# Optimization experiments

Measured on AMD Instinct MI355X. Metric: run time of the kernel, lower is better.

Reference implementation:

```python
import jax, jax.numpy as jnp
import numpy as np
from jax import lax

N_CLASSES = 10
N_EXPERTS = 45  # 10 choose 2
EPS = 1e-5

# lookup table: (i1, i2) with i1 < i2 -> flat expert id (matches nested loop order)
_tbl = np.zeros((N_CLASSES, N_CLASSES), dtype=np.int32)
_k = 0
for _i1 in range(N_CLASSES):
    for _i2 in range(_i1 + 1, N_CLASSES):
        _tbl[_i1, _i2] = _k
        _k += 1
PAIR_TABLE = jnp.asarray(_tbl)


def _downscale(x):
    # AvgPool2d(3, stride=3) on 28x28 -> 9x9 (floor: uses top-left 27x27)
    B = x.shape[0]
    return x[:, :, :27, :27].reshape(B, 1, 9, 3, 9, 3).mean(axis=(3, 5))


def _bn_eval(h, gamma, beta, mean, var):
    scale = gamma * lax.rsqrt(var + EPS)
    return h * scale[None, :, None, None] + (beta - mean * scale)[None, :, None, None]


def _stage1(x, w1, b1, g1, be1, m1, v1, fcw1, fcb1):
    xd = _downscale(x)                                         # [B,1,9,9]
    h = lax.conv_general_dilated(xd, w1, (1, 1), 'VALID',
                                 dimension_numbers=('NCHW', 'OIHW', 'NCHW'))
    h = h + b1[None, :, None, None]                            # [B,20,7,7]
    h = _bn_eval(h, g1, be1, m1, v1)
    h = jax.nn.relu(h)
    B = h.shape[0]
    h = h[:, :, :6, :6].reshape(B, 20, 3, 2, 3, 2).max(axis=(3, 5))  # maxpool2 -> [B,20,3,3]
    h = h.reshape(B, 180)
    return h @ fcw1.T + fcb1                                   # [B,10] raw logits


def reference(x, w1, b1, g1, be1, m1, v1, fcw1, fcb1,
              w2, b2, g2, be2, m2, v2, fcw2, fcb2):
    B = x.shape[0]
    logits1 = _stage1(x, w1, b1, g1, be1, m1, v1, fcw1, fcb1)  # [B,10]
    ls1 = jax.nn.log_softmax(logits1, axis=1)

    # routing: top-2 class indices, sorted ascending, -> pairwise expert id
    top2 = jnp.sort(jnp.argsort(ls1, axis=1)[:, -2:], axis=1)  # [B,2]
    idx0, idx1 = top2[:, 0], top2[:, 1]
    eid = PAIR_TABLE[idx0, idx1]                               # [B]

    # stage 2 (TinyNet2) with per-example gathered expert params
    xd = _downscale(x)                                         # [B,1,9,9]
    # extract 5x5 conv patches (valid, stride 1): output spatial 5x5
    patches = jnp.stack([xd[:, 0, i:i + 5, j:j + 5]
                         for i in range(5) for j in range(5)], axis=1)  # [B,25,5,5]
    Wsel = w2.reshape(N_EXPERTS, 15, 25)[eid]                  # [B,15,25]
    h = jnp.einsum('bkhw,bok->bohw', patches, Wsel) + b2[eid][:, :, None, None]  # [B,15,5,5]
    scale = (g2 * lax.rsqrt(v2 + EPS))[eid]                    # [B,15]
    shift = (be2 - m2 * g2 * lax.rsqrt(v2 + EPS))[eid]
    h = h * scale[:, :, None, None] + shift[:, :, None, None]
    h = jax.nn.relu(h)
    h = h[:, :, :4, :4].reshape(B, 15, 2, 2, 2, 2).max(axis=(3, 5))  # [B,15,2,2]
    feat = h.reshape(B, 60)
    s2 = jnp.einsum('bf,bof->bo', feat, fcw2[eid]) + fcb2[eid]  # [B,2]

    # combine: scatter the two expert logits into the routed columns
    rows = jnp.arange(B)
    out = jnp.full((B, N_CLASSES), -100.0, dtype=logits1.dtype)
    out = out.at[rows, idx0].set(s2[:, 0]).at[rows, idx1].set(s2[:, 1])
    # eval-mode bypass: use stage1 raw logits if max log-prob > 0.3
    use1 = jnp.max(ls1, axis=1) > 0.3
    out = jnp.where(use1[:, None], logits1, out)
    out = jax.nn.log_softmax(out, axis=1)
    return (logits1, out)


def setup_inputs() -> dict:
    key = jax.random.key(0)
    ks = jax.random.split(key, 18)
    B = 65536
    s = 0.1
    return {
        'x': jax.random.normal(ks[0], (B, 1, 28, 28), dtype=jnp.float32),
        # stage1 (TinyNet, 20 kernels, k=3)
        'w1': jax.random.normal(ks[1], (20, 1, 3, 3), dtype=jnp.float32) * s,
        'b1': jax.random.normal(ks[2], (20,), dtype=jnp.float32) * s,
        'g1': jax.random.normal(ks[3], (20,), dtype=jnp.float32) * s + 1.0,
        'be1': jax.random.normal(ks[4], (20,), dtype=jnp.float32) * s,
        'm1': jax.random.normal(ks[5], (20,), dtype=jnp.float32) * s,
        'v1': jax.random.uniform(ks[6], (20,), dtype=jnp.float32) + 0.5,
        'fcw1': jax.random.normal(ks[7], (10, 180), dtype=jnp.float32) * s,
        'fcb1': jax.random.normal(ks[8], (10,), dtype=jnp.float32) * s,
        # 45 stacked stage2 experts (TinyNet2, 15 kernels, k=5)
        'w2': jax.random.normal(ks[9], (45, 15, 1, 5, 5), dtype=jnp.float32) * s,
        'b2': jax.random.normal(ks[10], (45, 15), dtype=jnp.float32) * s,
        'g2': jax.random.normal(ks[11], (45, 15), dtype=jnp.float32) * s + 1.0,
        'be2': jax.random.normal(ks[12], (45, 15), dtype=jnp.float32) * s,
        'm2': jax.random.normal(ks[13], (45, 15), dtype=jnp.float32) * s,
        'v2': jax.random.uniform(ks[14], (45, 15), dtype=jnp.float32) + 0.5,
        'fcw2': jax.random.normal(ks[15], (45, 2, 60), dtype=jnp.float32) * s,
        'fcb2': jax.random.normal(ks[16], (45, 2), dtype=jnp.float32) * s,
    }
```

## Files before the change

kernel.cpp:

```cpp
#include <hip/hip_runtime.h>
#include <cmath>

#define EPSF 1e-5f


__global__ __launch_bounds__(256) void setup_tables(
    const float* __restrict__ w1, const float* __restrict__ b1,
    const float* __restrict__ g1, const float* __restrict__ be1,
    const float* __restrict__ m1, const float* __restrict__ v1,
    const float* __restrict__ w2, const float* __restrict__ b2,
    const float* __restrict__ g2, const float* __restrict__ be2,
    const float* __restrict__ m2, const float* __restrict__ v2,
    const float* __restrict__ fcw2, const float* __restrict__ fcb2,
    float* __restrict__ ws)
{
  const int t  = blockIdx.x * blockDim.x + threadIdx.x;
  const int nt = gridDim.x * blockDim.x;
  float* W2F  = ws;
  float* B2F  = W2F + 18900;
  float* FC2  = W2F + 19576;
  float* FCB2 = FC2 + 5400;
  float* W1F  = FCB2 + 90;
  float* B1F  = W1F + 180;

  for (int idx = t; idx < 18900; idx += nt) {
    int kk = idx & 3, rest = idx >> 2;
    int e = rest % 45, ok4 = rest / 45;
    int k4 = ok4 % 7, o = ok4 / 7;
    int k = k4 * 4 + kk;
    float s = g2[e*15+o] / sqrtf(v2[e*15+o] + EPSF);
    W2F[idx] = (k < 25) ? w2[(e*15+o)*25 + k] * s : 0.0f;
  }
  for (int idx = t; idx < 675; idx += nt) {
    int e = idx % 45, o = idx / 45;
    float s = g2[e*15+o] / sqrtf(v2[e*15+o] + EPSF);
    B2F[idx] = b2[e*15+o]*s + be2[e*15+o] - m2[e*15+o]*s;
  }
  for (int idx = t; idx < 5400; idx += nt) {
    int kk = idx & 3, rest = idx >> 2;
    int e = rest % 45, t2 = rest / 45;
    int f4 = t2 % 15, oo = t2 / 15;
    FC2[idx] = fcw2[(e*2+oo)*60 + f4*4 + kk];
  }
  for (int idx = t; idx < 90; idx += nt) {
    int e = idx % 45, oo = idx / 45;
    FCB2[idx] = fcb2[e*2+oo];
  }
  for (int idx = t; idx < 180; idx += nt) {
    int ch = idx / 9;
    float s = g1[ch] / sqrtf(v1[ch] + EPSF);
    W1F[idx] = w1[idx] * s;
  }
  for (int idx = t; idx < 20; idx += nt) {
    float s = g1[idx] / sqrtf(v1[idx] + EPSF);
    B1F[idx] = b1[idx]*s + be1[idx] - m1[idx]*s;
  }
}

#define GETC(arr, k) ((k)%4==0 ? arr[(k)/4].x : (k)%4==1 ? arr[(k)/4].y : \
                      (k)%4==2 ? arr[(k)/4].z : arr[(k)/4].w)

__global__ __launch_bounds__(64, 1) void fused_k(
    const float* __restrict__ x,
    const float* __restrict__ ws,
    const float* __restrict__ fcw1, const float* __restrict__ fcb1,
    float* __restrict__ out, int B)
{
  const int b = blockIdx.x * 64 + threadIdx.x;
  if (b >= B) return;

  const float* W2F  = ws;
  const float* B2F  = W2F + 18900;
  const float* FC2  = W2F + 19576;
  const float* FCB2 = FC2 + 5400;
  const float* W1F  = FCB2 + 90;
  const float* B1F  = W1F + 180;

  float xd[81];
  const float* xb = x + (size_t)b * 784;
  #pragma unroll
  for (int r = 0; r < 9; r++) {
    float4 rowv[3][7];
    #pragma unroll
    for (int dr = 0; dr < 3; dr++) {
      const float4* rv = reinterpret_cast<const float4*>(xb + (3*r + dr) * 28);
      #pragma unroll
      for (int q = 0; q < 7; q++) rowv[dr][q] = rv[q];
    }
    #pragma unroll
    for (int c = 0; c < 9; c++) {
      float s = 0.0f;
      #pragma unroll
      for (int dr = 0; dr < 3; dr++)
        s += GETC(rowv[dr], 3*c) + GETC(rowv[dr], 3*c+1) + GETC(rowv[dr], 3*c+2);
      xd[r*9 + c] = s * (1.0f / 9.0f);
    }
  }

  float logits[10];
  #pragma unroll
  for (int c = 0; c < 10; c++) logits[c] = fcb1[c];

  #pragma unroll 1
  for (int ch = 0; ch < 20; ch++) {
    float w[9];
    #pragma unroll
    for (int k = 0; k < 9; k++) w[k] = W1F[ch*9 + k];
    float bb = B1F[ch];
    float feat[9];
    #pragma unroll
    for (int pr = 0; pr < 3; pr++) {
      #pragma unroll
      for (int pc = 0; pc < 3; pc++) {
        float c00 = bb, c01 = bb, c10 = bb, c11 = bb;
        #pragma unroll
        for (int dr = 0; dr < 3; dr++) {
          #pragma unroll
          for (int dc = 0; dc < 3; dc++) {
            float wk = w[dr*3 + dc];
            c00 = fmaf(xd[(2*pr+0+dr)*9 + 2*pc+0+dc], wk, c00);
            c01 = fmaf(xd[(2*pr+0+dr)*9 + 2*pc+1+dc], wk, c01);
            c10 = fmaf(xd[(2*pr+1+dr)*9 + 2*pc+0+dc], wk, c10);
            c11 = fmaf(xd[(2*pr+1+dr)*9 + 2*pc+1+dc], wk, c11);
          }
        }
        feat[pr*3+pc] = fmaxf(fmaxf(fmaxf(c00, c01), fmaxf(c10, c11)), 0.0f);
      }
    }
    #pragma unroll
    for (int c = 0; c < 10; c++) {
      float acc = logits[c];
      #pragma unroll
      for (int p = 0; p < 9; p++)
        acc = fmaf(feat[p], fcw1[c*180 + ch*9 + p], acc);
      logits[c] = acc;
    }
  }

  int i1 = 0; float v1m = logits[0];
  #pragma unroll
  for (int c = 1; c < 10; c++) { if (logits[c] >= v1m) { v1m = logits[c]; i1 = c; } }
  int i2 = 0; float v2m = -3.0e38f;
  #pragma unroll
  for (int c = 0; c < 10; c++) { if (c != i1 && logits[c] >= v2m) { v2m = logits[c]; i2 = c; } }
  int idx0 = i1 < i2 ? i1 : i2;
  int idx1 = i1 < i2 ? i2 : i1;
  int eid  = 8*idx0 - (idx0*(idx0-1))/2 + idx1 - 1;

  float mx = v1m;
  float sume = 0.0f;
  #pragma unroll
  for (int c = 0; c < 10; c++) sume += expf(logits[c] - mx);
  bool use1 = (-logf(sume)) > 0.3f;

  const float4* W2F4 = reinterpret_cast<const float4*>(W2F);
  const float4* FC24 = reinterpret_cast<const float4*>(FC2);

  float s2a = FCB2[eid], s2b = FCB2[45 + eid];

  float4 wv[7], fa, fb; float bias;
  #pragma unroll
  for (int k4 = 0; k4 < 7; k4++) wv[k4] = W2F4[k4*45 + eid];
  bias = B2F[eid];
  fa = FC24[eid];
  fb = FC24[15*45 + eid];

  #pragma unroll 1
  for (int o = 0; o < 15; o++) {
    float4 nwv[7], nfa, nfb; float nbias;
    if (o < 14) {
      #pragma unroll
      for (int k4 = 0; k4 < 7; k4++) nwv[k4] = W2F4[((o+1)*7 + k4)*45 + eid];
      nbias = B2F[(o+1)*45 + eid];
      nfa = FC24[(o+1)*45 + eid];
      nfb = FC24[(15 + o+1)*45 + eid];
    }
    float feat0 = 0.f, feat1 = 0.f, feat2 = 0.f, feat3 = 0.f;
    #pragma unroll
    for (int ph = 0; ph < 2; ph++) {
      #pragma unroll
      for (int pw = 0; pw < 2; pw++) {
        float c00 = bias, c01 = bias, c10 = bias, c11 = bias;
        #pragma unroll
        for (int i = 0; i < 5; i++) {
          #pragma unroll
          for (int j = 0; j < 5; j++) {
            float wk = GETC(wv, i*5 + j);
            c00 = fmaf(xd[(2*ph+0+i)*9 + 2*pw+0+j], wk, c00);
            c01 = fmaf(xd[(2*ph+0+i)*9 + 2*pw+1+j], wk, c01);
            c10 = fmaf(xd[(2*ph+1+i)*9 + 2*pw+0+j], wk, c10);
            c11 = fmaf(xd[(2*ph+1+i)*9 + 2*pw+1+j], wk, c11);
          }
        }
        float f = fmaxf(fmaxf(fmaxf(c00, c01), fmaxf(c10, c11)), 0.0f);
        if (ph == 0 && pw == 0) feat0 = f;
        else if (ph == 0)       feat1 = f;
        else if (pw == 0)       feat2 = f;
        else                    feat3 = f;
      }
    }
    s2a = fmaf(feat0, fa.x, fmaf(feat1, fa.y, fmaf(feat2, fa.z, fmaf(feat3, fa.w, s2a))));
    s2b = fmaf(feat0, fb.x, fmaf(feat1, fb.y, fmaf(feat2, fb.z, fmaf(feat3, fb.w, s2b))));
    if (o < 14) {
      #pragma unroll
      for (int k4 = 0; k4 < 7; k4++) wv[k4] = nwv[k4];
      bias = nbias; fa = nfa; fb = nfb;
    }
  }

  float o10[10];
  #pragma unroll
  for (int c = 0; c < 10; c++) {
    float v = -100.0f;
    v = (c == idx0) ? s2a : v;
    v = (c == idx1) ? s2b : v;
    o10[c] = use1 ? logits[c] : v;
  }
  float m2x = o10[0];
  #pragma unroll
  for (int c = 1; c < 10; c++) m2x = fmaxf(m2x, o10[c]);
  float se2 = 0.0f;
  #pragma unroll
  for (int c = 0; c < 10; c++) se2 += expf(o10[c] - m2x);
  float lse2 = m2x + logf(se2);

  size_t base = (size_t)b * 10;
  #pragma unroll
  for (int c = 0; c < 10; c++) out[base + c] = logits[c];
  #pragma unroll
  for (int c = 0; c < 10; c++) out[(size_t)B*10 + base + c] = o10[c] - lse2;
}

extern "C" void kernel_launch(void* const* d_in, const int* in_sizes, int n_in,
                              void* d_out, int out_size, void* d_ws, size_t ws_size,
                              hipStream_t stream) {
  const float* x    = (const float*)d_in[0];
  const float* w1   = (const float*)d_in[1];
  const float* b1   = (const float*)d_in[2];
  const float* g1   = (const float*)d_in[3];
  const float* be1  = (const float*)d_in[4];
  const float* m1   = (const float*)d_in[5];
  const float* v1   = (const float*)d_in[6];
  const float* fcw1 = (const float*)d_in[7];
  const float* fcb1 = (const float*)d_in[8];
  const float* w2   = (const float*)d_in[9];
  const float* b2   = (const float*)d_in[10];
  const float* g2   = (const float*)d_in[11];
  const float* be2  = (const float*)d_in[12];
  const float* m2   = (const float*)d_in[13];
  const float* v2   = (const float*)d_in[14];
  const float* fcw2 = (const float*)d_in[15];
  const float* fcb2 = (const float*)d_in[16];
  float* out = (float*)d_out;
  float* ws  = (float*)d_ws;
  const int B = in_sizes[0] / 784;

  setup_tables<<<80, 256, 0, stream>>>(w1, b1, g1, be1, m1, v1,
                                       w2, b2, g2, be2, m2, v2, fcw2, fcb2, ws);
  fused_k<<<(B + 63)/64, 64, 0, stream>>>(x, ws, fcw1, fcb1, out, B);
}
```

Before: 369.8 us.

## Split each sample across four lanes with shared-memory downscale and shuffle reductions

Each sample is now handled by four threads instead of one. The threads share the input downscale through LDS, split the stage-1 conv channels and the stage-2 expert output channels, and combine partial logits with xor shuffles. The fc1 weights are re-laid out in setup so they can be read with float4 loads, and the downscaled image is trimmed to the 8x8 region actually used. This is meant to cut per-thread register pressure and serial latency and to give the launch more waves. In exchange it duplicates the routing and softmax work across the four lanes and adds a block barrier.

```diff
diff --git a/kernel.cpp b/kernel.cpp
--- a/kernel.cpp
+++ b/kernel.cpp
@@ -3,6 +3,12 @@
 
 #define EPSF 1e-5f
 
+#define OFF_B2F   18900
+#define OFF_FC2   19576
+#define OFF_FCB2  24976
+#define OFF_W1P   25068
+#define OFF_FCW1R 25308
+#define OFF_B1F   27468
 
 __global__ __launch_bounds__(256) void setup_tables(
     const float* __restrict__ w1, const float* __restrict__ b1,
@@ -12,16 +18,18 @@
     const float* __restrict__ g2, const float* __restrict__ be2,
     const float* __restrict__ m2, const float* __restrict__ v2,
     const float* __restrict__ fcw2, const float* __restrict__ fcb2,
+    const float* __restrict__ fcw1,
     float* __restrict__ ws)
 {
   const int t  = blockIdx.x * blockDim.x + threadIdx.x;
   const int nt = gridDim.x * blockDim.x;
-  float* W2F  = ws;
-  float* B2F  = W2F + 18900;
-  float* FC2  = W2F + 19576;
-  float* FCB2 = FC2 + 5400;
-  float* W1F  = FCB2 + 90;
-  float* B1F  = W1F + 180;
+  float* W2F   = ws;
+  float* B2F   = ws + OFF_B2F;
+  float* FC2   = ws + OFF_FC2;
+  float* FCB2  = ws + OFF_FCB2;
+  float* W1P   = ws + OFF_W1P;
+  float* FCW1R = ws + OFF_FCW1R;
+  float* B1F   = ws + OFF_B1F;
 
   for (int idx = t; idx < 18900; idx += nt) {
     int kk = idx & 3, rest = idx >> 2;
@@ -46,10 +54,15 @@
     int e = idx % 45, oo = idx / 45;
     FCB2[idx] = fcb2[e*2+oo];
   }
-  for (int idx = t; idx < 180; idx += nt) {
-    int ch = idx / 9;
+  for (int idx = t; idx < 240; idx += nt) {
+    int j = idx % 12, ch = idx / 12;
     float s = g1[ch] / sqrtf(v1[ch] + EPSF);
-    W1F[idx] = w1[idx] * s;
+    W1P[idx] = (j < 9) ? w1[ch*9 + j] * s : 0.0f;
+  }
+  for (int idx = t; idx < 2160; idx += nt) {
+    int c = idx % 12, r2 = idx / 12;
+    int pp = r2 % 9, ch = r2 / 9;
+    FCW1R[idx] = (c < 10) ? fcw1[c*180 + ch*9 + pp] : 0.0f;
   }
   for (int idx = t; idx < 20; idx += nt) {
     float s = g1[idx] / sqrtf(v1[idx] + EPSF);
@@ -60,53 +73,76 @@
 #define GETC(arr, k) ((k)%4==0 ? arr[(k)/4].x : (k)%4==1 ? arr[(k)/4].y : \
                       (k)%4==2 ? arr[(k)/4].z : arr[(k)/4].w)
 
-__global__ __launch_bounds__(64, 1) void fused_k(
+__global__ __launch_bounds__(256, 3) void fused_k(
     const float* __restrict__ x,
     const float* __restrict__ ws,
-    const float* __restrict__ fcw1, const float* __restrict__ fcb1,
+    const float* __restrict__ fcb1,
     float* __restrict__ out, int B)
 {
-  const int b = blockIdx.x * 64 + threadIdx.x;
-  if (b >= B) return;
-
-  const float* W2F  = ws;
-  const float* B2F  = W2F + 18900;
-  const float* FC2  = W2F + 19576;
-  const float* FCB2 = FC2 + 5400;
-  const float* W1F  = FCB2 + 90;
-  const float* B1F  = W1F + 180;
-
-  float xd[81];
-  const float* xb = x + (size_t)b * 784;
-  #pragma unroll
-  for (int r = 0; r < 9; r++) {
-    float4 rowv[3][7];
+  __shared__ float xds[64 * 68];
+
+  const int t  = threadIdx.x;
+  const int p  = t & 3;
+  const int sl = t >> 2;
+  const int b  = blockIdx.x * 64 + sl;
+  const bool valid = (b < B);
+
+  const float* W2F   = ws;
+  const float* B2F   = ws + OFF_B2F;
+  const float* FC2   = ws + OFF_FC2;
+  const float* FCB2  = ws + OFF_FCB2;
+  const float* W1P   = ws + OFF_W1P;
+  const float* FCW1R = ws + OFF_FCW1R;
+  const float* B1F   = ws + OFF_B1F;
+
+  if (valid) {
+    const float* xb = x + (size_t)b * 784;
     #pragma unroll
-    for (int dr = 0; dr < 3; dr++) {
-      const float4* rv = reinterpret_cast<const float4*>(xb + (3*r + dr) * 28);
-      #pragma unroll
-      for (int q = 0; q < 7; q++) rowv[dr][q] = rv[q];
-    }
-    #pragma unroll
-    for (int c = 0; c < 9; c++) {
-      float s = 0.0f;
-      #pragma unroll
-      for (int dr = 0; dr < 3; dr++)
-        s += GETC(rowv[dr], 3*c) + GETC(rowv[dr], 3*c+1) + GETC(rowv[dr], 3*c+2);
-      xd[r*9 + c] = s * (1.0f / 9.0f);
-    }
+    for (int ri = 0; ri < 2; ri++) {
+      const int r = 2*p + ri;
+      float4 rowv[3][6];
+      #pragma unroll
+      for (int dr = 0; dr < 3; dr++) {
+        const float4* rv = reinterpret_cast<const float4*>(xb + (3*r + dr) * 28);
+        #pragma unroll
+        for (int q = 0; q < 6; q++) rowv[dr][q] = rv[q];
+      }
+      float d[8];
+      #pragma unroll
+      for (int c = 0; c < 8; c++) {
+        float s = 0.0f;
+        #pragma unroll
+        for (int dr = 0; dr < 3; dr++)
+          s += GETC(rowv[dr], 3*c) + GETC(rowv[dr], 3*c+1) + GETC(rowv[dr], 3*c+2);
+        d[c] = s * (1.0f / 9.0f);
+      }
+      float4* dst = reinterpret_cast<float4*>(&xds[sl*68 + r*8]);
+      dst[0] = make_float4(d[0], d[1], d[2], d[3]);
+      dst[1] = make_float4(d[4], d[5], d[6], d[7]);
+    }
+  }
+  __syncthreads();
+
+  float xd[64];
+  #pragma unroll
+  for (int r = 0; r < 8; r++) {
+    const float4* src = reinterpret_cast<const float4*>(&xds[sl*68 + r*8]);
+    float4 a = src[0], bq = src[1];
+    xd[r*8+0]=a.x;  xd[r*8+1]=a.y;  xd[r*8+2]=a.z;  xd[r*8+3]=a.w;
+    xd[r*8+4]=bq.x; xd[r*8+5]=bq.y; xd[r*8+6]=bq.z; xd[r*8+7]=bq.w;
   }
 
   float logits[10];
   #pragma unroll
-  for (int c = 0; c < 10; c++) logits[c] = fcb1[c];
+  for (int c = 0; c < 10; c++) logits[c] = 0.0f;
 
   #pragma unroll 1
-  for (int ch = 0; ch < 20; ch++) {
-    float w[9];
-    #pragma unroll
-    for (int k = 0; k < 9; k++) w[k] = W1F[ch*9 + k];
-    float bb = B1F[ch];
+  for (int ci = 0; ci < 5; ci++) {
+    const int ch = p*5 + ci;
+    const float4* wp = reinterpret_cast<const float4*>(W1P + ch*12);
+    float4 w0 = wp[0], w1v = wp[1], w2v = wp[2];
+    const float w_[9] = {w0.x,w0.y,w0.z,w0.w,w1v.x,w1v.y,w1v.z,w1v.w,w2v.x};
+    const float bb = B1F[ch];
     float feat[9];
     #pragma unroll
     for (int pr = 0; pr < 3; pr++) {
@@ -117,24 +153,40 @@
         for (int dr = 0; dr < 3; dr++) {
           #pragma unroll
           for (int dc = 0; dc < 3; dc++) {
-            float wk = w[dr*3 + dc];
-            c00 = fmaf(xd[(2*pr+0+dr)*9 + 2*pc+0+dc], wk, c00);
-            c01 = fmaf(xd[(2*pr+0+dr)*9 + 2*pc+1+dc], wk, c01);
-            c10 = fmaf(xd[(2*pr+1+dr)*9 + 2*pc+0+dc], wk, c10);
-            c11 = fmaf(xd[(2*pr+1+dr)*9 + 2*pc+1+dc], wk, c11);
+            float wk = w_[dr*3 + dc];
+            c00 = fmaf(xd[(2*pr+0+dr)*8 + 2*pc+0+dc], wk, c00);
+            c01 = fmaf(xd[(2*pr+0+dr)*8 + 2*pc+1+dc], wk, c01);
+            c10 = fmaf(xd[(2*pr+1+dr)*8 + 2*pc+0+dc], wk, c10);
+            c11 = fmaf(xd[(2*pr+1+dr)*8 + 2*pc+1+dc], wk, c11);
           }
         }
         feat[pr*3+pc] = fmaxf(fmaxf(fmaxf(c00, c01), fmaxf(c10, c11)), 0.0f);
       }
     }
     #pragma unroll
-    for (int c = 0; c < 10; c++) {
-      float acc = logits[c];
-      #pragma unroll
-      for (int p = 0; p < 9; p++)
-        acc = fmaf(feat[p], fcw1[c*180 + ch*9 + p], acc);
-      logits[c] = acc;
-    }
+    for (int pp = 0; pp < 9; pp++) {
+      const float4* f4 = reinterpret_cast<const float4*>(FCW1R + (ch*9 + pp)*12);
+      float4 f0 = f4[0], f1 = f4[1], f2 = f4[2];
+      const float fv = feat[pp];
+      logits[0] = fmaf(fv, f0.x, logits[0]);
+      logits[1] = fmaf(fv, f0.y, logits[1]);
+      logits[2] = fmaf(fv, f0.z, logits[2]);
+      logits[3] = fmaf(fv, f0.w, logits[3]);
+      logits[4] = fmaf(fv, f1.x, logits[4]);
+      logits[5] = fmaf(fv, f1.y, logits[5]);
+      logits[6] = fmaf(fv, f1.z, logits[6]);
+      logits[7] = fmaf(fv, f1.w, logits[7]);
+      logits[8] = fmaf(fv, f2.x, logits[8]);
+      logits[9] = fmaf(fv, f2.y, logits[9]);
+    }
+  }
+
+  #pragma unroll
+  for (int c = 0; c < 10; c++) {
+    float v = logits[c];
+    v += __shfl_xor(v, 1);
+    v += __shfl_xor(v, 2);
+    logits[c] = v + fcb1[c];
   }
 
   int i1 = 0; float v1m = logits[0];
@@ -143,70 +195,62 @@
   int i2 = 0; float v2m = -3.0e38f;
   #pragma unroll
   for (int c = 0; c < 10; c++) { if (c != i1 && logits[c] >= v2m) { v2m = logits[c]; i2 = c; } }
-  int idx0 = i1 < i2 ? i1 : i2;
-  int idx1 = i1 < i2 ? i2 : i1;
-  int eid  = 8*idx0 - (idx0*(idx0-1))/2 + idx1 - 1;
-
-  float mx = v1m;
+  const int idx0 = i1 < i2 ? i1 : i2;
+  const int idx1 = i1 < i2 ? i2 : i1;
+  int eid = 8*idx0 - (idx0*(idx0-1))/2 + idx1 - 1;
+  eid = eid < 0 ? 0 : (eid > 44 ? 44 : eid);
+
   float sume = 0.0f;
   #pragma unroll
-  for (int c = 0; c < 10; c++) sume += expf(logits[c] - mx);
-  bool use1 = (-logf(sume)) > 0.3f;
+  for (int c = 0; c < 10; c++) sume += expf(logits[c] - v1m);
+  const bool use1 = (-logf(sume)) > 0.3f;
 
   const float4* W2F4 = reinterpret_cast<const float4*>(W2F);
   const float4* FC24 = reinterpret_cast<const float4*>(FC2);
-
-  float s2a = FCB2[eid], s2b = FCB2[45 + eid];
-
-  float4 wv[7], fa, fb; float bias;
-  #pragma unroll
-  for (int k4 = 0; k4 < 7; k4++) wv[k4] = W2F4[k4*45 + eid];
-  bias = B2F[eid];
-  fa = FC24[eid];
-  fb = FC24[15*45 + eid];
+  float s2a = 0.0f, s2b = 0.0f;
 
   #pragma unroll 1
-  for (int o = 0; o < 15; o++) {
-    float4 nwv[7], nfa, nfb; float nbias;
-    if (o < 14) {
-      #pragma unroll
-      for (int k4 = 0; k4 < 7; k4++) nwv[k4] = W2F4[((o+1)*7 + k4)*45 + eid];
-      nbias = B2F[(o+1)*45 + eid];
-      nfa = FC24[(o+1)*45 + eid];
-      nfb = FC24[(15 + o+1)*45 + eid];
-    }
-    float feat0 = 0.f, feat1 = 0.f, feat2 = 0.f, feat3 = 0.f;
-    #pragma unroll
-    for (int ph = 0; ph < 2; ph++) {
-      #pragma unroll
-      for (int pw = 0; pw < 2; pw++) {
-        float c00 = bias, c01 = bias, c10 = bias, c11 = bias;
+  for (int oi = 0; oi < 4; oi++) {
+    const int o = p + 4*oi;
+    if (o < 15) {
+      float4 wv[7];
+      #pragma unroll
+      for (int k4 = 0; k4 < 7; k4++) wv[k4] = W2F4[(o*7 + k4)*45 + eid];
+      const float bias = B2F[o*45 + eid];
+      const float4 fa = FC24[o*45 + eid];
+      const float4 fb = FC24[(15 + o)*45 + eid];
+      float feat0 = 0.f, feat1 = 0.f, feat2 = 0.f, feat3 = 0.f;
+      #pragma unroll
+      for (int ph = 0; ph < 2; ph++) {
         #pragma unroll
-        for (int i = 0; i < 5; i++) {
+        for (int pw = 0; pw < 2; pw++) {
+          float c00 = bias, c01 = bias, c10 = bias, c11 = bias;
           #pragma unroll
-          for (int j = 0; j < 5; j++) {
-            float wk = GETC(wv, i*5 + j);
-            c00 = fmaf(xd[(2*ph+0+i)*9 + 2*pw+0+j], wk, c00);
-            c01 = fmaf(xd[(2*ph+0+i)*9 + 2*pw+1+j], wk, c01);
-            c10 = fmaf(xd[(2*ph+1+i)*9 + 2*pw+0+j], wk, c10);
-            c11 = fmaf(xd[(2*ph+1+i)*9 + 2*pw+1+j], wk, c11);
+          for (int i = 0; i < 5; i++) {
+            #pragma unroll
+            for (int j = 0; j < 5; j++) {
+              float wk = GETC(wv, i*5 + j);
+              c00 = fmaf(xd[(2*ph+0+i)*8 + 2*pw+0+j], wk, c00);
+              c01 = fmaf(xd[(2*ph+0+i)*8 + 2*pw+1+j], wk, c01);
+              c10 = fmaf(xd[(2*ph+1+i)*8 + 2*pw+0+j], wk, c10);
+              c11 = fmaf(xd[(2*ph+1+i)*8 + 2*pw+1+j], wk, c11);
+            }
           }
+          float f = fmaxf(fmaxf(fmaxf(c00, c01), fmaxf(c10, c11)), 0.0f);
+          if (ph == 0 && pw == 0) feat0 = f;
+          else if (ph == 0)       feat1 = f;
+          else if (pw == 0)       feat2 = f;
+          else                    feat3 = f;
         }
-        float f = fmaxf(fmaxf(fmaxf(c00, c01), fmaxf(c10, c11)), 0.0f);
-        if (ph == 0 && pw == 0) feat0 = f;
-        else if (ph == 0)       feat1 = f;
-        else if (pw == 0)       feat2 = f;
-        else                    feat3 = f;
       }
-    }
-    s2a = fmaf(feat0, fa.x, fmaf(feat1, fa.y, fmaf(feat2, fa.z, fmaf(feat3, fa.w, s2a))));
-    s2b = fmaf(feat0, fb.x, fmaf(feat1, fb.y, fmaf(feat2, fb.z, fmaf(feat3, fb.w, s2b))));
-    if (o < 14) {
-      #pragma unroll
-      for (int k4 = 0; k4 < 7; k4++) wv[k4] = nwv[k4];
-      bias = nbias; fa = nfa; fb = nfb;
-    }
-  }
+      s2a = fmaf(feat0, fa.x, fmaf(feat1, fa.y, fmaf(feat2, fa.z, fmaf(feat3, fa.w, s2a))));
+      s2b = fmaf(feat0, fb.x, fmaf(feat1, fb.y, fmaf(feat2, fb.z, fmaf(feat3, fb.w, s2b))));
+    }
+  }
+  s2a += __shfl_xor(s2a, 1); s2a += __shfl_xor(s2a, 2);
+  s2b += __shfl_xor(s2b, 1); s2b += __shfl_xor(s2b, 2);
+  s2a += FCB2[eid];
+  s2b += FCB2[45 + eid];
 
   float o10[10];
   #pragma unroll
@@ -222,13 +266,24 @@
   float se2 = 0.0f;
   #pragma unroll
   for (int c = 0; c < 10; c++) se2 += expf(o10[c] - m2x);
-  float lse2 = m2x + logf(se2);
-
-  size_t base = (size_t)b * 10;
-  #pragma unroll
-  for (int c = 0; c < 10; c++) out[base + c] = logits[c];
-  #pragma unroll
-  for (int c = 0; c < 10; c++) out[(size_t)B*10 + base + c] = o10[c] - lse2;
+  const float lse2 = m2x + logf(se2);
+
+  if (valid) {
+    const size_t base = (size_t)b * 10;
+    if (p == 0) {
+      #pragma unroll
+      for (int c = 0; c < 5; c++) out[base + c] = logits[c];
+    } else if (p == 1) {
+      #pragma unroll
+      for (int c = 5; c < 10; c++) out[base + c] = logits[c];
+    } else if (p == 2) {
+      #pragma unroll
+      for (int c = 0; c < 5; c++) out[(size_t)B*10 + base + c] = o10[c] - lse2;
+    } else {
+      #pragma unroll
+      for (int c = 5; c < 10; c++) out[(size_t)B*10 + base + c] = o10[c] - lse2;
+    }
+  }
 }
 
 extern "C" void kernel_launch(void* const* d_in, const int* in_sizes, int n_in,
@@ -256,6 +311,6 @@
   const int B = in_sizes[0] / 784;
 
   setup_tables<<<80, 256, 0, stream>>>(w1, b1, g1, be1, m1, v1,
-                                       w2, b2, g2, be2, m2, v2, fcw2, fcb2, ws);
-  fused_k<<<(B + 63)/64, 64, 0, stream>>>(x, ws, fcw1, fcb1, out, B);
+                                       w2, b2, g2, be2, m2, v2, fcw2, fcb2, fcw1, ws);
+  fused_k<<<(B + 63)/64, 256, 0, stream>>>(x, ws, fcb1, out, B);
 }
```

Result: no change. 376.7 us (+1.8%).

## Stage input images through LDS with coalesced loads and staged output stores

Applied to the files above, without the earlier changes.

Each block of 128 threads now loads its images cooperatively: 16 threads per image, 8 images per chunk, using coalesced float4 reads with register prefetch of the next chunk. The 3x3 average pooling is done from LDS into a padded 8x8 layout per sample, since only the top-left 8x8 of the 9x9 map is used. The expert bias and fc bias are packed into the unused pad slots of the weight float4s, which removes separate gathers. Outputs go through LDS so full blocks can write them as coalesced float4 stores. In exchange the kernel uses about 56 KB of shared memory and extra barriers, which limits occupancy.

```diff
diff --git a/kernel.cpp b/kernel.cpp
--- a/kernel.cpp
+++ b/kernel.cpp
@@ -3,6 +3,9 @@
 
 #define EPSF 1e-5f
 
+#define OFF_FC2 18900
+#define OFF_W1F 24300
+#define OFF_B1F 24480
 
 __global__ __launch_bounds__(256) void setup_tables(
     const float* __restrict__ w1, const float* __restrict__ b1,
@@ -16,12 +19,10 @@
 {
   const int t  = blockIdx.x * blockDim.x + threadIdx.x;
   const int nt = gridDim.x * blockDim.x;
-  float* W2F  = ws;
-  float* B2F  = W2F + 18900;
-  float* FC2  = W2F + 19576;
-  float* FCB2 = FC2 + 5400;
-  float* W1F  = FCB2 + 90;
-  float* B1F  = W1F + 180;
+  float* W2F = ws;
+  float* FC2 = ws + OFF_FC2;
+  float* W1F = ws + OFF_W1F;
+  float* B1F = ws + OFF_B1F;
 
   for (int idx = t; idx < 18900; idx += nt) {
     int kk = idx & 3, rest = idx >> 2;
@@ -29,12 +30,12 @@
     int k4 = ok4 % 7, o = ok4 / 7;
     int k = k4 * 4 + kk;
     float s = g2[e*15+o] / sqrtf(v2[e*15+o] + EPSF);
-    W2F[idx] = (k < 25) ? w2[(e*15+o)*25 + k] * s : 0.0f;
-  }
-  for (int idx = t; idx < 675; idx += nt) {
-    int e = idx % 45, o = idx / 45;
-    float s = g2[e*15+o] / sqrtf(v2[e*15+o] + EPSF);
-    B2F[idx] = b2[e*15+o]*s + be2[e*15+o] - m2[e*15+o]*s;
+    float v;
+    if (k < 25)       v = w2[(e*15+o)*25 + k] * s;
+    else if (k == 25) v = b2[e*15+o]*s + be2[e*15+o] - m2[e*15+o]*s;
+    else if (k == 26) v = (o == 0) ? fcb2[e*2 + 0] : 0.0f;
+    else              v = (o == 0) ? fcb2[e*2 + 1] : 0.0f;
+    W2F[idx] = v;
   }
   for (int idx = t; idx < 5400; idx += nt) {
     int kk = idx & 3, rest = idx >> 2;
@@ -42,10 +43,6 @@
     int f4 = t2 % 15, oo = t2 / 15;
     FC2[idx] = fcw2[(e*2+oo)*60 + f4*4 + kk];
   }
-  for (int idx = t; idx < 90; idx += nt) {
-    int e = idx % 45, oo = idx / 45;
-    FCB2[idx] = fcb2[e*2+oo];
-  }
   for (int idx = t; idx < 180; idx += nt) {
     int ch = idx / 9;
     float s = g1[ch] / sqrtf(v1[ch] + EPSF);
@@ -60,41 +57,86 @@
 #define GETC(arr, k) ((k)%4==0 ? arr[(k)/4].x : (k)%4==1 ? arr[(k)/4].y : \
                       (k)%4==2 ? arr[(k)/4].z : arr[(k)/4].w)
 
-__global__ __launch_bounds__(64, 1) void fused_k(
+#define NS     128
+#define CHS    8
+#define NCH    (NS/CHS)
+#define T_RAW  8704
+#define SSTR4  169
+
+__global__ __launch_bounds__(128, 1) void fused_k(
     const float* __restrict__ x,
     const float* __restrict__ ws,
     const float* __restrict__ fcw1, const float* __restrict__ fcb1,
     float* __restrict__ out, int B)
 {
-  const int b = blockIdx.x * 64 + threadIdx.x;
-  if (b >= B) return;
-
-  const float* W2F  = ws;
-  const float* B2F  = W2F + 18900;
-  const float* FC2  = W2F + 19576;
-  const float* FCB2 = FC2 + 5400;
-  const float* W1F  = FCB2 + 90;
-  const float* B1F  = W1F + 180;
-
-  float xd[81];
-  const float* xb = x + (size_t)b * 784;
-  #pragma unroll
-  for (int r = 0; r < 9; r++) {
-    float4 rowv[3][7];
-    #pragma unroll
-    for (int dr = 0; dr < 3; dr++) {
-      const float4* rv = reinterpret_cast<const float4*>(xb + (3*r + dr) * 28);
-      #pragma unroll
-      for (int q = 0; q < 7; q++) rowv[dr][q] = rv[q];
-    }
-    #pragma unroll
-    for (int c = 0; c < 9; c++) {
-      float s = 0.0f;
-      #pragma unroll
-      for (int dr = 0; dr < 3; dr++)
-        s += GETC(rowv[dr], 3*c) + GETC(rowv[dr], 3*c+1) + GETC(rowv[dr], 3*c+2);
-      xd[r*9 + c] = s * (1.0f / 9.0f);
-    }
+  __shared__ float lds[14112];
+
+  const int t  = threadIdx.x;
+  const int B0 = blockIdx.x * NS;
+
+  const float* W1F = ws + OFF_W1F;
+  const float* B1F = ws + OFF_B1F;
+
+  const int cs = t >> 4;
+  const int ti = t & 15;
+  const float4* xg = reinterpret_cast<const float4*>(x);
+  float4* RAW4 = reinterpret_cast<float4*>(&lds[T_RAW]);
+
+  float4 pre[11];
+  {
+    const size_t bs = (size_t)(B0 + cs);
+    #pragma unroll
+    for (int k = 0; k < 11; k++) {
+      const int q = ti + 16*k;
+      if (q < 168 && (int)bs < B) pre[k] = xg[bs*196 + q];
+    }
+  }
+
+  #pragma unroll 1
+  for (int c = 0; c < NCH; c++) {
+    __syncthreads();
+    #pragma unroll
+    for (int k = 0; k < 11; k++) {
+      const int q = ti + 16*k;
+      if (q < 168) RAW4[cs*SSTR4 + q] = pre[k];
+    }
+    if (c < NCH-1) {
+      const size_t bs = (size_t)(B0 + (c+1)*CHS + cs);
+      #pragma unroll
+      for (int k = 0; k < 11; k++) {
+        const int q = ti + 16*k;
+        if (q < 168 && (int)bs < B) pre[k] = xg[bs*196 + q];
+      }
+    }
+    __syncthreads();
+    {
+      const int orow = ti >> 1, cp = ti & 1;
+      float a0 = 0.f, a1 = 0.f, a2 = 0.f, a3 = 0.f;
+      #pragma unroll
+      for (int dr = 0; dr < 3; dr++) {
+        const float4* rp = reinterpret_cast<const float4*>(
+            &lds[T_RAW + cs*SSTR4*4 + (3*orow + dr)*28 + 12*cp]);
+        float4 q0 = rp[0], q1 = rp[1], q2 = rp[2];
+        a0 += q0.x + q0.y + q0.z;
+        a1 += q0.w + q1.x + q1.y;
+        a2 += q1.z + q1.w + q2.x;
+        a3 += q2.y + q2.z + q2.w;
+      }
+      float4* dst = reinterpret_cast<float4*>(
+          &lds[(c*CHS + cs)*68 + orow*8 + 4*cp]);
+      *dst = make_float4(a0*(1.0f/9.0f), a1*(1.0f/9.0f),
+                         a2*(1.0f/9.0f), a3*(1.0f/9.0f));
+    }
+  }
+  __syncthreads();
+
+  float xd[64];
+  #pragma unroll
+  for (int r = 0; r < 8; r++) {
+    const float4* src = reinterpret_cast<const float4*>(&lds[t*68 + r*8]);
+    float4 a = src[0], bq = src[1];
+    xd[r*8+0]=a.x;  xd[r*8+1]=a.y;  xd[r*8+2]=a.z;  xd[r*8+3]=a.w;
+    xd[r*8+4]=bq.x; xd[r*8+5]=bq.y; xd[r*8+6]=bq.z; xd[r*8+7]=bq.w;
   }
 
   float logits[10];
@@ -118,10 +160,10 @@
           #pragma unroll
           for (int dc = 0; dc < 3; dc++) {
             float wk = w[dr*3 + dc];
-            c00 = fmaf(xd[(2*pr+0+dr)*9 + 2*pc+0+dc], wk, c00);
-            c01 = fmaf(xd[(2*pr+0+dr)*9 + 2*pc+1+dc], wk, c01);
-            c10 = fmaf(xd[(2*pr+1+dr)*9 + 2*pc+0+dc], wk, c10);
-            c11 = fmaf(xd[(2*pr+1+dr)*9 + 2*pc+1+dc], wk, c11);
+            c00 = fmaf(xd[(2*pr+0+dr)*8 + 2*pc+0+dc], wk, c00);
+            c01 = fmaf(xd[(2*pr+0+dr)*8 + 2*pc+1+dc], wk, c01);
+            c10 = fmaf(xd[(2*pr+1+dr)*8 + 2*pc+0+dc], wk, c10);
+            c11 = fmaf(xd[(2*pr+1+dr)*8 + 2*pc+1+dc], wk, c11);
           }
         }
         feat[pr*3+pc] = fmaxf(fmaxf(fmaxf(c00, c01), fmaxf(c10, c11)), 0.0f);
@@ -143,38 +185,39 @@
   int i2 = 0; float v2m = -3.0e38f;
   #pragma unroll
   for (int c = 0; c < 10; c++) { if (c != i1 && logits[c] >= v2m) { v2m = logits[c]; i2 = c; } }
-  int idx0 = i1 < i2 ? i1 : i2;
-  int idx1 = i1 < i2 ? i2 : i1;
-  int eid  = 8*idx0 - (idx0*(idx0-1))/2 + idx1 - 1;
+  const int idx0 = i1 < i2 ? i1 : i2;
+  const int idx1 = i1 < i2 ? i2 : i1;
+  int eid = 8*idx0 - (idx0*(idx0-1))/2 + idx1 - 1;
+  eid = eid < 0 ? 0 : (eid > 44 ? 44 : eid);
 
   float mx = v1m;
   float sume = 0.0f;
   #pragma unroll
   for (int c = 0; c < 10; c++) sume += expf(logits[c] - mx);
-  bool use1 = (-logf(sume)) > 0.3f;
-
-  const float4* W2F4 = reinterpret_cast<const float4*>(W2F);
-  const float4* FC24 = reinterpret_cast<const float4*>(FC2);
-
-  float s2a = FCB2[eid], s2b = FCB2[45 + eid];
-
-  float4 wv[7], fa, fb; float bias;
+  const bool use1 = (-logf(sume)) > 0.3f;
+
+  const float4* W2F4 = reinterpret_cast<const float4*>(ws);
+  const float4* FC24 = reinterpret_cast<const float4*>(ws + OFF_FC2);
+
+  float4 wv[7], fa, fb;
   #pragma unroll
   for (int k4 = 0; k4 < 7; k4++) wv[k4] = W2F4[k4*45 + eid];
-  bias = B2F[eid];
   fa = FC24[eid];
   fb = FC24[15*45 + eid];
 
+  float s2a = wv[6].z;
+  float s2b = wv[6].w;
+
   #pragma unroll 1
   for (int o = 0; o < 15; o++) {
-    float4 nwv[7], nfa, nfb; float nbias;
+    float4 nwv[7], nfa, nfb;
     if (o < 14) {
       #pragma unroll
       for (int k4 = 0; k4 < 7; k4++) nwv[k4] = W2F4[((o+1)*7 + k4)*45 + eid];
-      nbias = B2F[(o+1)*45 + eid];
       nfa = FC24[(o+1)*45 + eid];
       nfb = FC24[(15 + o+1)*45 + eid];
     }
+    const float bias = wv[6].y;
     float feat0 = 0.f, feat1 = 0.f, feat2 = 0.f, feat3 = 0.f;
     #pragma unroll
     for (int ph = 0; ph < 2; ph++) {
@@ -186,10 +229,10 @@
           #pragma unroll
           for (int j = 0; j < 5; j++) {
             float wk = GETC(wv, i*5 + j);
-            c00 = fmaf(xd[(2*ph+0+i)*9 + 2*pw+0+j], wk, c00);
-            c01 = fmaf(xd[(2*ph+0+i)*9 + 2*pw+1+j], wk, c01);
-            c10 = fmaf(xd[(2*ph+1+i)*9 + 2*pw+0+j], wk, c10);
-            c11 = fmaf(xd[(2*ph+1+i)*9 + 2*pw+1+j], wk, c11);
+            c00 = fmaf(xd[(2*ph+0+i)*8 + 2*pw+0+j], wk, c00);
+            c01 = fmaf(xd[(2*ph+0+i)*8 + 2*pw+1+j], wk, c01);
+            c10 = fmaf(xd[(2*ph+1+i)*8 + 2*pw+0+j], wk, c10);
+            c11 = fmaf(xd[(2*ph+1+i)*8 + 2*pw+1+j], wk, c11);
           }
         }
         float f = fmaxf(fmaxf(fmaxf(c00, c01), fmaxf(c10, c11)), 0.0f);
@@ -204,7 +247,7 @@
     if (o < 14) {
       #pragma unroll
       for (int k4 = 0; k4 < 7; k4++) wv[k4] = nwv[k4];
-      bias = nbias; fa = nfa; fb = nfb;
+      fa = nfa; fb = nfb;
     }
   }
 
@@ -222,13 +265,30 @@
   float se2 = 0.0f;
   #pragma unroll
   for (int c = 0; c < 10; c++) se2 += expf(o10[c] - m2x);
-  float lse2 = m2x + logf(se2);
-
-  size_t base = (size_t)b * 10;
-  #pragma unroll
-  for (int c = 0; c < 10; c++) out[base + c] = logits[c];
-  #pragma unroll
-  for (int c = 0; c < 10; c++) out[(size_t)B*10 + base + c] = o10[c] - lse2;
+  const float lse2 = m2x + logf(se2);
+
+  #pragma unroll
+  for (int c = 0; c < 10; c++) lds[T_RAW + t*10 + c] = logits[c];
+  #pragma unroll
+  for (int c = 0; c < 10; c++) lds[T_RAW + 1280 + t*10 + c] = o10[c] - lse2;
+  __syncthreads();
+
+  if (B0 + NS <= B) {
+    const float4* l4 = reinterpret_cast<const float4*>(&lds[T_RAW]);
+    float4* o1 = reinterpret_cast<float4*>(out + (size_t)B0*10);
+    float4* o2 = reinterpret_cast<float4*>(out + (size_t)B*10 + (size_t)B0*10);
+    #pragma unroll
+    for (int k = 0; k < 3; k++) {
+      const int f = t + 128*k;
+      if (f < 320) { o1[f] = l4[f]; o2[f] = l4[320 + f]; }
+    }
+  } else if (B0 + t < B) {
+    const size_t base = (size_t)(B0 + t)*10;
+    #pragma unroll
+    for (int c = 0; c < 10; c++) out[base + c] = lds[T_RAW + t*10 + c];
+    #pragma unroll
+    for (int c = 0; c < 10; c++) out[(size_t)B*10 + base + c] = lds[T_RAW + 1280 + t*10 + c];
+  }
 }
 
 extern "C" void kernel_launch(void* const* d_in, const int* in_sizes, int n_in,
@@ -257,5 +317,5 @@
 
   setup_tables<<<80, 256, 0, stream>>>(w1, b1, g1, be1, m1, v1,
                                        w2, b2, g2, be2, m2, v2, fcw2, fcb2, ws);
-  fused_k<<<(B + 63)/64, 64, 0, stream>>>(x, ws, fcw1, fcb1, out, B);
+  fused_k<<<(B + NS - 1)/NS, 128, 0, stream>>>(x, ws, fcw1, fcb1, out, B);
 }
```

Measured after the change: 380.3 us. +2.8%, slower.
